# Optimization experiments

Measured on AMD Instinct MI355X. Metric: run time of the kernel, lower is better.

The kernel has to match this reference:

```python
import jax, jax.numpy as jnp
import numpy as np

HIDDEN = 50


def _lstm_layer(x_tbi, w_ih, w_hh, b_ih, b_hh):
    """One LSTM layer, PyTorch gate order (i, f, g, o).
    x_tbi: [T, B, in]; returns h sequence [T, B, H]."""
    B = x_tbi.shape[1]
    H = w_hh.shape[1]
    # Precompute input projections for all timesteps at once (one big GEMM).
    x_proj = jnp.einsum('tbi,gi->tbg', x_tbi, w_ih) + b_ih + b_hh  # [T, B, 4H]

    def step(carry, xp):
        h, c = carry
        gates = xp + h @ w_hh.T  # [B, 4H]
        i, f, g, o = jnp.split(gates, 4, axis=-1)
        i = jax.nn.sigmoid(i)
        f = jax.nn.sigmoid(f)
        g = jnp.tanh(g)
        o = jax.nn.sigmoid(o)
        c = f * c + i * g
        h = o * jnp.tanh(c)
        return (h, c), h

    h0 = jnp.zeros((B, H), dtype=x_tbi.dtype)
    c0 = jnp.zeros((B, H), dtype=x_tbi.dtype)
    _, hs = jax.lax.scan(step, (h0, c0), x_proj)
    return hs  # [T, B, H]


def setup_inputs() -> dict:
    key = jax.random.key(0)
    ks = jax.random.split(key, 12)
    B, T, I, H = 2048, 512, 12, HIDDEN
    s_in = 1.0 / np.sqrt(H)  # PyTorch LSTM init scale
    inp = {
        'x': jax.random.normal(ks[0], (B, T, I), dtype=jnp.float32),
        'w_ih0': jax.random.uniform(ks[1], (4 * H, I), jnp.float32, -s_in, s_in),
        'w_hh0': jax.random.uniform(ks[2], (4 * H, H), jnp.float32, -s_in, s_in),
        'b_ih0': jax.random.uniform(ks[3], (4 * H,), jnp.float32, -s_in, s_in),
        'b_hh0': jax.random.uniform(ks[4], (4 * H,), jnp.float32, -s_in, s_in),
        'w_ih1': jax.random.uniform(ks[5], (4 * H, H), jnp.float32, -s_in, s_in),
        'w_hh1': jax.random.uniform(ks[6], (4 * H, H), jnp.float32, -s_in, s_in),
        'b_ih1': jax.random.uniform(ks[7], (4 * H,), jnp.float32, -s_in, s_in),
        'b_hh1': jax.random.uniform(ks[8], (4 * H,), jnp.float32, -s_in, s_in),
        'w_out': jax.random.uniform(ks[9], (1, H), jnp.float32, -s_in, s_in),
        'b_out': jax.random.uniform(ks[10], (1,), jnp.float32, -s_in, s_in),
    }
    return inp


def reference(x, w_ih0, w_hh0, b_ih0, b_hh0, w_ih1, w_hh1, b_ih1, b_hh1, w_out, b_out):
    # x: [B, T, I] (batch_first). Scan works over leading time axis.
    x_tbi = jnp.transpose(x, (1, 0, 2))  # [T, B, I]
    h1 = _lstm_layer(x_tbi, w_ih0, w_hh0, b_ih0, b_hh0)  # [T, B, H]
    h2 = _lstm_layer(h1, w_ih1, w_hh1, b_ih1, b_hh1)     # [T, B, H]
    last = h2[-1]                                         # r_out[:, -1, :] -> [B, H]
    logits = last @ w_out.T + b_out                       # [B, 1]
    return jax.nn.sigmoid(logits)
```

## Files before the change

### kernel.cpp

```cpp
#include <hip/hip_runtime.h>

#define TT   512
#define BI   12
#define HH   50
#define BB   8
#define BTOT 2048
#define LOG2E 1.4426950408889634f


typedef _Float16 half8 __attribute__((ext_vector_type(8)));
typedef float    f4    __attribute__((ext_vector_type(4)));

__device__ __forceinline__ float sigm_(float v) {
    return __builtin_amdgcn_rcpf(1.f + __builtin_amdgcn_exp2f(v * (-LOG2E)));
}
__device__ __forceinline__ float tanh_(float v) {
    return 1.f - 2.f * __builtin_amdgcn_rcpf(1.f + __builtin_amdgcn_exp2f(v * (2.f * LOG2E)));
}
__device__ __forceinline__ float dppmerge_(float a0, float a1) {
    int r = __builtin_amdgcn_update_dpp(__builtin_bit_cast(int, a0),
                                        __builtin_bit_cast(int, a1),
                                        0x128, 0xF, 0xC, false);
    return __builtin_bit_cast(float, r);
}

__launch_bounds__(1024)
__global__ void lstm2_kernel(const float* __restrict__ x,
                             const float* __restrict__ w_ih0, const float* __restrict__ w_hh0,
                             const float* __restrict__ b_ih0, const float* __restrict__ b_hh0,
                             const float* __restrict__ w_ih1, const float* __restrict__ w_hh1,
                             const float* __restrict__ b_ih1, const float* __restrict__ b_hh1,
                             const float* __restrict__ w_out, const float* __restrict__ b_out,
                             float* __restrict__ out)
{
    const int tid   = threadIdx.x;
    const int wv    = tid >> 6;
    const int lane  = tid & 63;
    const int layer = wv >> 3;
    const int w8    = wv & 7;
    const int b0    = blockIdx.x * BB;
    const int t0     = (w8 < 5) ? 2 * w8 : (5 + w8);
    const int ntiles = (w8 < 5) ? 2 : 1;

    __shared__ __align__(16) _Float16 B0s[2][64  * 16];
    __shared__ __align__(16) _Float16 B1s[2][128 * 16];

    const int m = lane & 15;
    const int q = lane >> 4;
    half8 af[2][4];
    #pragma unroll
    for (int s = 0; s < 2; s++) {
        #pragma unroll
        for (int kb = 0; kb < 4; kb++) {
            #pragma unroll
            for (int j = 0; j < 8; j++) {
                float v = 0.f;
                if (s < ntiles && (layer == 1 || kb < 2)) {
                    const int T  = t0 + s;
                    const int u  = T * 4 + (m >> 2);
                    const int g  = m & 3;
                    const int kg = kb * 32 + q * 8 + j;
                    if (u < HH) {
                        const int r = g * HH + u;
                        if (layer == 0) {
                            if      (kg < 12)  v = w_ih0[r * BI + kg];
                            else if (kg < 62)  v = w_hh0[r * HH + (kg - 12)];
                            else if (kg == 62) v = b_ih0[r] + b_hh0[r];
                        } else {
                            if      (kg < 50)  v = w_ih1[r * HH + kg];
                            else if (kg < 64)  v = 0.f;
                            else if (kg < 114) v = w_hh1[r * HH + (kg - 64)];
                            else if (kg == 114) v = b_ih1[r] + b_hh1[r];
                        }
                    }
                }
                af[s][kb][j] = (_Float16)v;
            }
        }
    }

    for (int i = tid; i < 2 * 64 * 16;  i += 1024) (&B0s[0][0])[i] = (_Float16)0.f;
    for (int i = tid; i < 2 * 128 * 16; i += 1024) (&B1s[0][0])[i] = (_Float16)0.f;
    __syncthreads();
    if (tid < 16) {
        B0s[0][7  * 128 + tid * 8 + 6] = (_Float16)1.f;
        B0s[1][7  * 128 + tid * 8 + 6] = (_Float16)1.f;
        B1s[0][14 * 128 + tid * 8 + 2] = (_Float16)1.f;
        B1s[1][14 * 128 + tid * 8 + 2] = (_Float16)1.f;
    }
    const int xb = tid / 12, xi = tid - xb * 12;
    const int xoff = (xi >> 3) * 128 + xb * 8 + (xi & 7);
    const size_t xbase = ((size_t)(b0 + xb) * TT) * BI + xi;
    if (tid < 96)
        B0s[0][xoff] = (_Float16)x[xbase];
    __syncthreads();

    const int n16  = lane & 15;
    const int slot = n16 >> 3;
    const int bcol = n16 & 7;
    const int u_m  = (t0 + slot) * 4 + q;
    const bool wvalid = (u_m < HH) && (slot == 0 || ntiles == 2);
    float cm = 0.f;

    const _Float16* rdA[2] = { (layer ? &B1s[0][0] : &B0s[0][0]) + lane * 8,
                               (layer ? &B1s[1][0] : &B0s[1][0]) + lane * 8 };
    const int k0 = 12 + u_m;
    const int k1 = 64 + u_m;
    const int offA = layer ? ((k1 >> 3) * 128 + bcol * 8 + (k1 & 7))
                           : ((k0 >> 3) * 128 + bcol * 8 + (k0 & 7));
    const int offB = (u_m >> 3) * 128 + bcol * 8 + (u_m & 7);
    _Float16* wAp[2] = { (layer ? &B1s[0][0] : &B0s[0][0]) + offA,
                         (layer ? &B1s[1][0] : &B0s[1][0]) + offA };
    _Float16* wBp[2] = { &B1s[0][0] + offB, &B1s[1][0] + offB };
    _Float16* xdp[2] = { &B0s[0][0] + xoff, &B0s[1][0] + xoff };

    const float* xq = x + xbase + BI;
    float xhold = 0.f;
    if (tid < 96) xhold = *xq;
    xq += BI;

#define STEP(P, DOL0, DOL1, DOST, DOLD)                                       \
  {                                                                           \
    float xnew = 0.f;                                                         \
    if ((DOLD) && tid < 96) xnew = *xq;                                       \
    if ((DOST) && tid < 96) *xdp[1 - (P)] = (_Float16)xhold;                  \
    if ((layer == 0) ? (DOL0) : (DOL1)) {                                     \
      f4 acc0 = {0.f, 0.f, 0.f, 0.f}, acc1 = {0.f, 0.f, 0.f, 0.f};            \
      const _Float16* Bp = rdA[P];                                            \
      if (layer == 0) {                                                       \
        const half8 bf0 = *(const half8*)(Bp);                                \
        const half8 bf1 = *(const half8*)(Bp + 512);                          \
        acc0 = __builtin_amdgcn_mfma_f32_16x16x32_f16(af[0][0], bf0, acc0, 0, 0, 0); \
        if (ntiles > 1)                                                       \
          acc1 = __builtin_amdgcn_mfma_f32_16x16x32_f16(af[1][0], bf0, acc1, 0, 0, 0); \
        acc0 = __builtin_amdgcn_mfma_f32_16x16x32_f16(af[0][1], bf1, acc0, 0, 0, 0); \
        if (ntiles > 1)                                                       \
          acc1 = __builtin_amdgcn_mfma_f32_16x16x32_f16(af[1][1], bf1, acc1, 0, 0, 0); \
      } else {                                                                \
        f4 acc0b = {0.f, 0.f, 0.f, 0.f}, acc1b = {0.f, 0.f, 0.f, 0.f};        \
        const half8 bf0 = *(const half8*)(Bp);                                \
        const half8 bf1 = *(const half8*)(Bp + 512);                          \
        const half8 bf2 = *(const half8*)(Bp + 1024);                         \
        const half8 bf3 = *(const half8*)(Bp + 1536);                         \
        acc0  = __builtin_amdgcn_mfma_f32_16x16x32_f16(af[0][0], bf0, acc0,  0, 0, 0); \
        if (ntiles > 1)                                                       \
          acc1  = __builtin_amdgcn_mfma_f32_16x16x32_f16(af[1][0], bf0, acc1,  0, 0, 0); \
        acc0b = __builtin_amdgcn_mfma_f32_16x16x32_f16(af[0][1], bf1, acc0b, 0, 0, 0); \
        if (ntiles > 1)                                                       \
          acc1b = __builtin_amdgcn_mfma_f32_16x16x32_f16(af[1][1], bf1, acc1b, 0, 0, 0); \
        acc0  = __builtin_amdgcn_mfma_f32_16x16x32_f16(af[0][2], bf2, acc0,  0, 0, 0); \
        if (ntiles > 1)                                                       \
          acc1  = __builtin_amdgcn_mfma_f32_16x16x32_f16(af[1][2], bf2, acc1,  0, 0, 0); \
        acc0b = __builtin_amdgcn_mfma_f32_16x16x32_f16(af[0][3], bf3, acc0b, 0, 0, 0); \
        if (ntiles > 1)                                                       \
          acc1b = __builtin_amdgcn_mfma_f32_16x16x32_f16(af[1][3], bf3, acc1b, 0, 0, 0); \
        acc0 += acc0b;                                                        \
        acc1 += acc1b;                                                        \
      }                                                                       \
      f4 am;                                                                  \
      _Pragma("unroll")                                                       \
      for (int i = 0; i < 4; i++) am[i] = dppmerge_(acc0[i], acc1[i]);        \
      const float iv = sigm_(am[0]);                                          \
      const float fv = sigm_(am[1]);                                          \
      const float gv = tanh_(am[2]);                                          \
      const float ov = sigm_(am[3]);                                          \
      cm = fv * cm + iv * gv;                                                 \
      const float h = ov * tanh_(cm);                                         \
      if (wvalid) {                                                           \
        const _Float16 hh = (_Float16)h;                                      \
        *wAp[1 - (P)] = hh;                                                   \
        if (layer == 0) *wBp[1 - (P)] = hh;                                   \
      }                                                                       \
    }                                                                         \
    if (DOLD) { xhold = xnew; xq += BI; }                                     \
    __syncthreads();                                                          \
  }

    STEP(0, 1, 0, 1, 1)
    STEP(1, 1, 1, 1, 1)
    #pragma unroll 1
    for (int it = 0; it < 254; ++it) {
        STEP(0, 1, 1, 1, 1)
        STEP(1, 1, 1, 1, 1)
    }
    STEP(0, 1, 1, 1, 0)
    STEP(1, 1, 1, 0, 0)
    STEP(0, 0, 1, 0, 0)
#undef STEP

    if (tid < BB) {
        float s = b_out[0];
        #pragma unroll
        for (int u = 0; u < HH; u++) {
            const int kk = 64 + u;
            s += w_out[u] * (float)B1s[1][(kk >> 3) * 128 + tid * 8 + (kk & 7)];
        }
        out[b0 + tid] = sigm_(s);
    }
}

extern "C" void kernel_launch(void* const* d_in, const int* in_sizes, int n_in,
                              void* d_out, int out_size, void* d_ws, size_t ws_size,
                              hipStream_t stream) {
    const float* x     = (const float*)d_in[0];
    const float* w_ih0 = (const float*)d_in[1];
    const float* w_hh0 = (const float*)d_in[2];
    const float* b_ih0 = (const float*)d_in[3];
    const float* b_hh0 = (const float*)d_in[4];
    const float* w_ih1 = (const float*)d_in[5];
    const float* w_hh1 = (const float*)d_in[6];
    const float* b_ih1 = (const float*)d_in[7];
    const float* b_hh1 = (const float*)d_in[8];
    const float* w_out = (const float*)d_in[9];
    const float* b_out = (const float*)d_in[10];
    float* out = (float*)d_out;

    dim3 grid(BTOT / BB);
    dim3 block(1024);
    lstm2_kernel<<<grid, block, 0, stream>>>(x, w_ih0, w_hh0, b_ih0, b_hh0,
                                             w_ih1, w_hh1, b_ih1, b_hh1,
                                             w_out, b_out, out);
}
```

Baseline: 381.6 us.

## Share layer-0 h buffer with layer 1, fold activation scales into weights

Reorders the layer-0 K layout to put h first and x after it. Layer 1 now reads its h1 input straight from the layer-0 buffer, so layer 0 writes h only once and the duplicate write into the layer-1 buffer goes away. The layer-1 buffer shrinks to hold only h2 plus the bias row. The -log2e and 2*log2e activation scales are folded into the fp16 weights to drop a multiply per gate, and the MFMA accumulation is reordered to start from zero. Pre-scaling in fp16 slightly changes rounding, and the bias row moved to k=126, which must line up with the 1.0 entry in the layer-1 buffer.

```diff
diff --git a/kernel.cpp b/kernel.cpp
--- a/kernel.cpp
+++ b/kernel.cpp
@@ -11,6 +11,12 @@
 typedef _Float16 half8 __attribute__((ext_vector_type(8)));
 typedef float    f4    __attribute__((ext_vector_type(4)));
 
+__device__ __forceinline__ float sigmE_(float u) {
+    return __builtin_amdgcn_rcpf(1.f + __builtin_amdgcn_exp2f(u));
+}
+__device__ __forceinline__ float tanhE_(float u) {
+    return 1.f - 2.f * __builtin_amdgcn_rcpf(1.f + __builtin_amdgcn_exp2f(u));
+}
 __device__ __forceinline__ float sigm_(float v) {
     return __builtin_amdgcn_rcpf(1.f + __builtin_amdgcn_exp2f(v * (-LOG2E)));
 }
@@ -42,8 +48,8 @@
     const int t0     = (w8 < 5) ? 2 * w8 : (5 + w8);
     const int ntiles = (w8 < 5) ? 2 : 1;
 
-    __shared__ __align__(16) _Float16 B0s[2][64  * 16];
-    __shared__ __align__(16) _Float16 B1s[2][128 * 16];
+    __shared__ __align__(16) _Float16 B0s[2][64 * 16];
+    __shared__ __align__(16) _Float16 B1s[2][64 * 16];
 
     const int m = lane & 15;
     const int q = lane >> 4;
@@ -63,15 +69,15 @@
                     if (u < HH) {
                         const int r = g * HH + u;
                         if (layer == 0) {
-                            if      (kg < 12)  v = w_ih0[r * BI + kg];
-                            else if (kg < 62)  v = w_hh0[r * HH + (kg - 12)];
+                            if      (kg < 50)  v = w_hh0[r * HH + kg];
+                            else if (kg < 62)  v = w_ih0[r * BI + (kg - 50)];
                             else if (kg == 62) v = b_ih0[r] + b_hh0[r];
                         } else {
-                            if      (kg < 50)  v = w_ih1[r * HH + kg];
-                            else if (kg < 64)  v = 0.f;
-                            else if (kg < 114) v = w_hh1[r * HH + (kg - 64)];
-                            else if (kg == 114) v = b_ih1[r] + b_hh1[r];
+                            if      (kg < 50)               v = w_ih1[r * HH + kg];
+                            else if (kg >= 64 && kg < 114)  v = w_hh1[r * HH + (kg - 64)];
+                            else if (kg == 126)             v = b_ih1[r] + b_hh1[r];
                         }
+                        v *= (g == 2) ? (2.f * LOG2E) : (-LOG2E);
                     }
                 }
                 af[s][kb][j] = (_Float16)v;
@@ -79,17 +85,20 @@
         }
     }
 
-    for (int i = tid; i < 2 * 64 * 16;  i += 1024) (&B0s[0][0])[i] = (_Float16)0.f;
-    for (int i = tid; i < 2 * 128 * 16; i += 1024) (&B1s[0][0])[i] = (_Float16)0.f;
+    for (int i = tid; i < 2 * 64 * 16; i += 1024) {
+        (&B0s[0][0])[i] = (_Float16)0.f;
+        (&B1s[0][0])[i] = (_Float16)0.f;
+    }
     __syncthreads();
     if (tid < 16) {
-        B0s[0][7  * 128 + tid * 8 + 6] = (_Float16)1.f;
-        B0s[1][7  * 128 + tid * 8 + 6] = (_Float16)1.f;
-        B1s[0][14 * 128 + tid * 8 + 2] = (_Float16)1.f;
-        B1s[1][14 * 128 + tid * 8 + 2] = (_Float16)1.f;
+        B0s[0][7 * 128 + tid * 8 + 6] = (_Float16)1.f;
+        B0s[1][7 * 128 + tid * 8 + 6] = (_Float16)1.f;
+        B1s[0][7 * 128 + tid * 8 + 6] = (_Float16)1.f;
+        B1s[1][7 * 128 + tid * 8 + 6] = (_Float16)1.f;
     }
     const int xb = tid / 12, xi = tid - xb * 12;
-    const int xoff = (xi >> 3) * 128 + xb * 8 + (xi & 7);
+    const int xrow = 50 + xi;
+    const int xoff = (xrow >> 3) * 128 + xb * 8 + (xrow & 7);
     const size_t xbase = ((size_t)(b0 + xb) * TT) * BI + xi;
     if (tid < 96)
         B0s[0][xoff] = (_Float16)x[xbase];
@@ -102,17 +111,14 @@
     const bool wvalid = (u_m < HH) && (slot == 0 || ntiles == 2);
     float cm = 0.f;
 
-    const _Float16* rdA[2] = { (layer ? &B1s[0][0] : &B0s[0][0]) + lane * 8,
-                               (layer ? &B1s[1][0] : &B0s[1][0]) + lane * 8 };
-    const int k0 = 12 + u_m;
-    const int k1 = 64 + u_m;
-    const int offA = layer ? ((k1 >> 3) * 128 + bcol * 8 + (k1 & 7))
-                           : ((k0 >> 3) * 128 + bcol * 8 + (k0 & 7));
-    const int offB = (u_m >> 3) * 128 + bcol * 8 + (u_m & 7);
+    const _Float16* rd0[2] = { &B0s[0][0] + lane * 8, &B0s[1][0] + lane * 8 };
+    const _Float16* rd1[2] = { &B1s[0][0] + lane * 8, &B1s[1][0] + lane * 8 };
+    const int offA = (u_m >> 3) * 128 + bcol * 8 + (u_m & 7);
     _Float16* wAp[2] = { (layer ? &B1s[0][0] : &B0s[0][0]) + offA,
                          (layer ? &B1s[1][0] : &B0s[1][0]) + offA };
-    _Float16* wBp[2] = { &B1s[0][0] + offB, &B1s[1][0] + offB };
     _Float16* xdp[2] = { &B0s[0][0] + xoff, &B0s[1][0] + xoff };
+
+    const f4 fzero = {0.f, 0.f, 0.f, 0.f};
 
     const float* xq = x + xbase + BI;
     float xhold = 0.f;
@@ -125,52 +131,42 @@
     if ((DOLD) && tid < 96) xnew = *xq;                                       \
     if ((DOST) && tid < 96) *xdp[1 - (P)] = (_Float16)xhold;                  \
     if ((layer == 0) ? (DOL0) : (DOL1)) {                                     \
-      f4 acc0 = {0.f, 0.f, 0.f, 0.f}, acc1 = {0.f, 0.f, 0.f, 0.f};            \
-      const _Float16* Bp = rdA[P];                                            \
+      const half8 bf0 = *(const half8*)(rd0[P]);                              \
+      const half8 bf1 = *(const half8*)(rd0[P] + 512);                        \
+      f4 acc0, acc1 = fzero;                                                  \
       if (layer == 0) {                                                       \
-        const half8 bf0 = *(const half8*)(Bp);                                \
-        const half8 bf1 = *(const half8*)(Bp + 512);                          \
-        acc0 = __builtin_amdgcn_mfma_f32_16x16x32_f16(af[0][0], bf0, acc0, 0, 0, 0); \
-        if (ntiles > 1)                                                       \
-          acc1 = __builtin_amdgcn_mfma_f32_16x16x32_f16(af[1][0], bf0, acc1, 0, 0, 0); \
-        acc0 = __builtin_amdgcn_mfma_f32_16x16x32_f16(af[0][1], bf1, acc0, 0, 0, 0); \
-        if (ntiles > 1)                                                       \
-          acc1 = __builtin_amdgcn_mfma_f32_16x16x32_f16(af[1][1], bf1, acc1, 0, 0, 0); \
+        acc0 = __builtin_amdgcn_mfma_f32_16x16x32_f16(af[0][0], bf0, fzero, 0, 0, 0); \
+        acc0 = __builtin_amdgcn_mfma_f32_16x16x32_f16(af[0][1], bf1, acc0, 0, 0, 0);  \
+        if (ntiles > 1) {                                                     \
+          acc1 = __builtin_amdgcn_mfma_f32_16x16x32_f16(af[1][0], bf0, fzero, 0, 0, 0); \
+          acc1 = __builtin_amdgcn_mfma_f32_16x16x32_f16(af[1][1], bf1, acc1, 0, 0, 0);  \
+        }                                                                     \
       } else {                                                                \
-        f4 acc0b = {0.f, 0.f, 0.f, 0.f}, acc1b = {0.f, 0.f, 0.f, 0.f};        \
-        const half8 bf0 = *(const half8*)(Bp);                                \
-        const half8 bf1 = *(const half8*)(Bp + 512);                          \
-        const half8 bf2 = *(const half8*)(Bp + 1024);                         \
-        const half8 bf3 = *(const half8*)(Bp + 1536);                         \
-        acc0  = __builtin_amdgcn_mfma_f32_16x16x32_f16(af[0][0], bf0, acc0,  0, 0, 0); \
-        if (ntiles > 1)                                                       \
-          acc1  = __builtin_amdgcn_mfma_f32_16x16x32_f16(af[1][0], bf0, acc1,  0, 0, 0); \
-        acc0b = __builtin_amdgcn_mfma_f32_16x16x32_f16(af[0][1], bf1, acc0b, 0, 0, 0); \
-        if (ntiles > 1)                                                       \
-          acc1b = __builtin_amdgcn_mfma_f32_16x16x32_f16(af[1][1], bf1, acc1b, 0, 0, 0); \
-        acc0  = __builtin_amdgcn_mfma_f32_16x16x32_f16(af[0][2], bf2, acc0,  0, 0, 0); \
-        if (ntiles > 1)                                                       \
-          acc1  = __builtin_amdgcn_mfma_f32_16x16x32_f16(af[1][2], bf2, acc1,  0, 0, 0); \
-        acc0b = __builtin_amdgcn_mfma_f32_16x16x32_f16(af[0][3], bf3, acc0b, 0, 0, 0); \
-        if (ntiles > 1)                                                       \
-          acc1b = __builtin_amdgcn_mfma_f32_16x16x32_f16(af[1][3], bf3, acc1b, 0, 0, 0); \
-        acc0 += acc0b;                                                        \
-        acc1 += acc1b;                                                        \
+        const half8 bf2 = *(const half8*)(rd1[P]);                            \
+        const half8 bf3 = *(const half8*)(rd1[P] + 512);                      \
+        f4 a0  = __builtin_amdgcn_mfma_f32_16x16x32_f16(af[0][0], bf0, fzero, 0, 0, 0); \
+        f4 a0b = __builtin_amdgcn_mfma_f32_16x16x32_f16(af[0][1], bf1, fzero, 0, 0, 0); \
+        a0  = __builtin_amdgcn_mfma_f32_16x16x32_f16(af[0][2], bf2, a0,  0, 0, 0);      \
+        a0b = __builtin_amdgcn_mfma_f32_16x16x32_f16(af[0][3], bf3, a0b, 0, 0, 0);      \
+        acc0 = a0 + a0b;                                                      \
+        if (ntiles > 1) {                                                     \
+          f4 a1  = __builtin_amdgcn_mfma_f32_16x16x32_f16(af[1][0], bf0, fzero, 0, 0, 0); \
+          f4 a1b = __builtin_amdgcn_mfma_f32_16x16x32_f16(af[1][1], bf1, fzero, 0, 0, 0); \
+          a1  = __builtin_amdgcn_mfma_f32_16x16x32_f16(af[1][2], bf2, a1,  0, 0, 0);      \
+          a1b = __builtin_amdgcn_mfma_f32_16x16x32_f16(af[1][3], bf3, a1b, 0, 0, 0);      \
+          acc1 = a1 + a1b;                                                    \
+        }                                                                     \
       }                                                                       \
       f4 am;                                                                  \
       _Pragma("unroll")                                                       \
       for (int i = 0; i < 4; i++) am[i] = dppmerge_(acc0[i], acc1[i]);        \
-      const float iv = sigm_(am[0]);                                          \
-      const float fv = sigm_(am[1]);                                          \
-      const float gv = tanh_(am[2]);                                          \
-      const float ov = sigm_(am[3]);                                          \
+      const float iv = sigmE_(am[0]);                                         \
+      const float fv = sigmE_(am[1]);                                         \
+      const float gv = tanhE_(am[2]);                                         \
+      const float ov = sigmE_(am[3]);                                         \
       cm = fv * cm + iv * gv;                                                 \
       const float h = ov * tanh_(cm);                                         \
-      if (wvalid) {                                                           \
-        const _Float16 hh = (_Float16)h;                                      \
-        *wAp[1 - (P)] = hh;                                                   \
-        if (layer == 0) *wBp[1 - (P)] = hh;                                   \
-      }                                                                       \
+      if (wvalid) *wAp[1 - (P)] = (_Float16)h;                                \
     }                                                                         \
     if (DOLD) { xhold = xnew; xq += BI; }                                     \
     __syncthreads();                                                          \
@@ -192,8 +188,7 @@
         float s = b_out[0];
         #pragma unroll
         for (int u = 0; u < HH; u++) {
-            const int kk = 64 + u;
-            s += w_out[u] * (float)B1s[1][(kk >> 3) * 128 + tid * 8 + (kk & 7)];
+            s += w_out[u] * (float)B1s[1][(u >> 3) * 128 + tid * 8 + (u & 7)];
         }
         out[b0 + tid] = sigm_(s);
     }
```

After: 368.7 us. 3.4% less time.
